# Performance work log

Measured on AMD Instinct MI355X. Metric: run time of the kernel, lower is better.

## Reference

```python
import jax, jax.numpy as jnp
import numpy as np

# Quantization configuration mirroring the module-level constants in the source
INPUT_BIT, WEIGHT_BIT, OUTPUT_BIT, DAC_BIT, ADC_BIT = 8, 4, 8, 2, 8
N_SLICES = INPUT_BIT // DAC_BIT  # 4 bit-serial DAC slices of 2 bits each


def ste_round(v):
    # straight-through estimator round (fake-quant / LSQ style)
    return v + jax.lax.stop_gradient(jnp.round(v) - v)


def setup_inputs() -> dict:
    key = jax.random.key(0)
    k1, k2, k3 = jax.random.split(key, 3)
    B, IN_F, OUT_F = 32768, 1024, 1024
    x = jax.random.normal(k1, (B, IN_F), jnp.float32)
    weight = jax.random.normal(k2, (OUT_F, IN_F), jnp.float32) * 0.02
    bias = jax.random.normal(k3, (OUT_F,), jnp.float32) * 0.01
    # LSQ step sizes (learned scalars) for input / weight / output fake-quant
    s_x = jnp.float32(4.0 / 255.0)
    s_w = jnp.float32(0.01)
    s_o = jnp.float32(0.05)
    # per-output-column ADC gain (adc_adjust_mode='gain'); noise scales are 0 -> deterministic
    gain = jnp.ones((OUT_F,), jnp.float32)
    return {"x": x, "weight": weight, "bias": bias, "s_x": s_x, "s_w": s_w, "s_o": s_o, "gain": gain}


def reference(x, weight, bias, s_x, s_w, s_o, gain):
    QP_IN = float(2 ** INPUT_BIT - 1)                      # unsigned 8-bit activations
    QN_W, QP_W = float(-2 ** (WEIGHT_BIT - 1)), float(2 ** (WEIGHT_BIT - 1) - 1)  # signed 4-bit weights
    QN_A, QP_A = float(-2 ** (ADC_BIT - 1)), float(2 ** (ADC_BIT - 1) - 1)        # 8-bit ADC
    QN_O, QP_O = float(-2 ** (OUTPUT_BIT - 1)), float(2 ** (OUTPUT_BIT - 1) - 1)  # signed 8-bit output

    # --- input / weight fake quantization (LSQ) ---
    x_int = ste_round(jnp.clip(x / s_x, 0.0, QP_IN))       # [B, in_f] integer codes (float dtype)
    w_int = ste_round(jnp.clip(weight / s_w, QN_W, QP_W))  # [out_f, in_f]

    # ideal integer matmul result (differentiable path)
    ideal = jnp.matmul(x_int, w_int.T) * (s_x * s_w)       # [B, out_f]

    # --- bit-serial DAC slicing + per-slice ADC (hardware emulation, non-diff) ---
    xi = jax.lax.stop_gradient(x_int)
    wi = jax.lax.stop_gradient(w_int)
    g = jax.lax.stop_gradient(gain)                        # [out_f]
    base = float(2 ** DAC_BIT)
    acc = jnp.zeros((x.shape[0], weight.shape[0]), x.dtype)
    for i in range(N_SLICES):  # fixed small loop (4 slices)
        shift = base ** i
        sl = jnp.mod(jnp.floor(xi / shift), base)          # 2-bit slice in {0,1,2,3}
        partial = jnp.matmul(sl, wi.T)                     # analog MAC result [B, out_f]
        adc = jnp.clip(jnp.round(partial * g), QN_A, QP_A) / g  # ADC quant with column gain
        acc = acc + adc * shift
    out_cim = acc * (s_x * s_w)

    # straight-through: forward value = CIM-emulated, gradient = ideal path
    out = ideal + jax.lax.stop_gradient(out_cim - ideal) + bias

    # --- output fake quantization ---
    y = s_o * ste_round(jnp.clip(out / s_o, QN_O, QP_O))
    return y
```

## Files before the change

kernel.cpp:

```cpp
#pragma float_control(precise, on)
#include <hip/hip_runtime.h>
#include <stdint.h>


typedef int i32x4 __attribute__((ext_vector_type(4)));

#define MDIM   32768
#define KDIM   1024
#define NDIM   1024
#define ABLK   131072
#define AKTS   8192
#define BBLK   262144
#define BKTS   16384

__device__ __forceinline__ void gload16(const void* g, void* l) {
  __builtin_amdgcn_global_load_lds(
      (const __attribute__((address_space(1))) void*)g,
      (__attribute__((address_space(3))) void*)l,
      16, 0, 0);
}

__global__ __launch_bounds__(256) void quant_x_kernel(
    const float* __restrict__ x, const float* __restrict__ s_x_p,
    uint8_t* __restrict__ Aq, uint8_t* __restrict__ rowFlag) {
  const float rcp = 1.0f / s_x_p[0];
  const int tid = blockIdx.x * 256 + threadIdx.x;
  const int m   = tid >> 6;
  const int k16 = tid & 63;
  const float* xp = x + (size_t)m * KDIM + k16 * 16;
  float vv[16];
#pragma unroll
  for (int q = 0; q < 4; ++q) {
    const float4 v = *(const float4*)(xp + q * 4);
    vv[q * 4 + 0] = v.x; vv[q * 4 + 1] = v.y; vv[q * 4 + 2] = v.z; vv[q * 4 + 3] = v.w;
  }
  int c[16];
  bool anyAmb = false;
#pragma unroll
  for (int j = 0; j < 16; ++j) {
    const float t  = vv[j] * rcp;
    const float tc = fminf(fmaxf(t, 0.0f), 255.0f);
    const float kf = rintf(tc);
    c[j] = (int)kf;
    const float d = 0.5f - fabsf(tc - kf);
    anyAmb = anyAmb || (d < 4e-7f * (tc + 1.0f));
  }
  if (anyAmb) rowFlag[m] = 1;
  const int bm  = m >> 5;
  const int g   = (m >> 2) & 7;
  const int fr4 = (m & 3) * 4;
  const int kt  = k16 >> 2, kl = k16 & 3;
  uint8_t* base = Aq + (size_t)bm * ABLK + kt * AKTS + (g << 10) + (kl * 16 + fr4) * 16;
#pragma unroll
  for (int s = 0; s < 4; ++s) {
    uint32_t w[4];
#pragma unroll
    for (int q = 0; q < 4; ++q) {
      w[q] =  (uint32_t)((c[q*4+0] >> (2*s)) & 3)
           | ((uint32_t)((c[q*4+1] >> (2*s)) & 3) << 8)
           | ((uint32_t)((c[q*4+2] >> (2*s)) & 3) << 16)
           | ((uint32_t)((c[q*4+3] >> (2*s)) & 3) << 24);
    }
    *(uint4*)(base + s * 16) = make_uint4(w[0], w[1], w[2], w[3]);
  }
}

__global__ __launch_bounds__(256) void quant_w_kernel(
    const float* __restrict__ wgt, const float* __restrict__ s_w_p,
    uint8_t* __restrict__ Bq, int* __restrict__ colInfo) {
  const float rcp = 1.0f / s_w_p[0];
  const int tid = blockIdx.x * 256 + threadIdx.x;
  const int n   = tid >> 6;
  const int k16 = tid & 63;
  const float* wp = wgt + (size_t)n * KDIM + k16 * 16;
  float vv[16];
#pragma unroll
  for (int q = 0; q < 4; ++q) {
    const float4 v = *(const float4*)(wp + q * 4);
    vv[q * 4 + 0] = v.x; vv[q * 4 + 1] = v.y; vv[q * 4 + 2] = v.z; vv[q * 4 + 3] = v.w;
  }
  uint32_t w[4];
#pragma unroll
  for (int q = 0; q < 4; ++q) w[q] = 0;
#pragma unroll
  for (int j = 0; j < 16; ++j) {
    const float t  = vv[j] * rcp;
    const float tc = fminf(fmaxf(t, -8.0f), 7.0f);
    const float kf = rintf(tc);
    const int   iv = (int)kf;
    const float fr = tc - kf;
    const float d  = 0.5f - fabsf(fr);
    if (d < 4e-7f * (fabsf(tc) + 1.0f)) {
      const int jj = k16 * 16 + j;
      colInfo[n] = (jj << 2) | ((fr > 0.0f) ? 2 : 0) | 1;
    }
    w[j >> 2] |= (uint32_t)((uint8_t)iv) << (8 * (j & 3));
  }
  const int bn  = n >> 8;
  const int rr  = n & 255;
  const int g   = rr >> 4;
  const int fr_ = rr & 15;
  const int kt  = k16 >> 2, kl = k16 & 3;
  uint8_t* dst = Bq + (size_t)bn * BBLK + kt * BKTS + (g << 10) + (kl * 16 + fr_) * 16;
  *(uint4*)dst = make_uint4(w[0], w[1], w[2], w[3]);
}

struct ChainOut { float kf; float tc; };
__device__ __forceinline__ ChainOut cim_chain(float p0, float p1, float p2, float p3,
                                              float bi, float sxsw, float rcp_so) {
#pragma clang fp contract(off)
  const float a0 = fminf(fmaxf(p0, -128.f), 127.f);
  const float a1 = fminf(fmaxf(p1, -128.f), 127.f);
  const float a2 = fminf(fmaxf(p2, -128.f), 127.f);
  const float a3 = fminf(fmaxf(p3, -128.f), 127.f);
  float acc_i = a0 + a1 * 4.f;
  acc_i = acc_i + a2 * 16.f;
  acc_i = acc_i + a3 * 64.f;
  float idl_i = p0 + p1 * 4.f;
  idl_i = idl_i + p2 * 16.f;
  idl_i = idl_i + p3 * 64.f;
  const float cim  = acc_i * sxsw;
  const float idea = idl_i * sxsw;
  float ov = idea + (cim - idea);
  ov = ov + bi;
  const float t  = ov * rcp_so;
  const float tc = fminf(fmaxf(t, -128.f), 127.f);
  ChainOut r; r.kf = rintf(tc); r.tc = tc; return r;
}

__global__ __launch_bounds__(512, 4) void gemm_cim(
    const uint8_t* __restrict__ Aq, const uint8_t* __restrict__ Bq,
    const float* __restrict__ bias, const float* __restrict__ gain,
    const float* __restrict__ s_x_p, const float* __restrict__ s_w_p,
    const float* __restrict__ s_o_p, const uint8_t* __restrict__ rowFlag,
    const int* __restrict__ colInfo, float* __restrict__ C) {
  __shared__ uint8_t sA[3][8192];
  __shared__ uint8_t sB[3][16384];

  const int t    = threadIdx.x;
  const int l    = ((int)blockIdx.x & 7) * 512 + ((int)blockIdx.x >> 3);
  const int bn   = l & 3;
  const int bm   = l >> 2;
  const int lane = t & 63;
  const int wv   = t >> 6;
  const int wr   = wv >> 2, wc = wv & 3;
  const int fr   = lane & 15, lk = lane >> 4;

  const uint8_t* gA = Aq + (size_t)bm * ABLK;
  const uint8_t* gB = Bq + (size_t)bn * BBLK;

  i32x4 acc[4][4];
#pragma unroll
  for (int i = 0; i < 4; ++i)
#pragma unroll
    for (int j = 0; j < 4; ++j) acc[i][j] = (i32x4){0, 0, 0, 0};

  const int lofs = lane * 16;
  const int o0 = t * 16, o1 = t * 16 + 8192;

  auto STAGE_ALL = [&](int kt, int bf) {
    gload16(gA + kt * AKTS + o0, sA[bf] + o0);
    gload16(gB + kt * BKTS + o0, sB[bf] + o0);
    gload16(gB + kt * BKTS + o1, sB[bf] + o1);
  };

  STAGE_ALL(0, 0);
  STAGE_ALL(1, 1);

  for (int kt = 0; kt < 16; ++kt) {
    const int bf = kt % 3;
    const int pf = (kt + 2) % 3;
    if (kt < 15) asm volatile("s_waitcnt vmcnt(3)" ::: "memory");
    else         asm volatile("s_waitcnt vmcnt(0)" ::: "memory");
    __builtin_amdgcn_sched_barrier(0);
    __builtin_amdgcn_s_barrier();
    if (kt + 2 < 16) STAGE_ALL(kt + 2, pf);

    i32x4 b0 = *(const i32x4*)(sB[bf] + ((wc * 4 + 0) << 10) + lofs);
    i32x4 b1 = *(const i32x4*)(sB[bf] + ((wc * 4 + 1) << 10) + lofs);
    i32x4 b2 = *(const i32x4*)(sB[bf] + ((wc * 4 + 2) << 10) + lofs);
    i32x4 b3 = *(const i32x4*)(sB[bf] + ((wc * 4 + 3) << 10) + lofs);
    __builtin_amdgcn_s_setprio(1);
#pragma unroll
    for (int mi = 0; mi < 4; ++mi) {
      i32x4 a = *(const i32x4*)(sA[bf] + ((wr * 4 + mi) << 10) + lofs);
      acc[mi][0] = __builtin_amdgcn_mfma_i32_16x16x64_i8(a, b0, acc[mi][0], 0, 0, 0);
      acc[mi][1] = __builtin_amdgcn_mfma_i32_16x16x64_i8(a, b1, acc[mi][1], 0, 0, 0);
      acc[mi][2] = __builtin_amdgcn_mfma_i32_16x16x64_i8(a, b2, acc[mi][2], 0, 0, 0);
      acc[mi][3] = __builtin_amdgcn_mfma_i32_16x16x64_i8(a, b3, acc[mi][3], 0, 0, 0);
    }
    __builtin_amdgcn_s_setprio(0);
  }

  {
#pragma clang fp contract(off)
    const float sxf = s_x_p[0], swf = s_w_p[0], sof = s_o_p[0];
    const float sxsw   = sxf * swf;
    const float rcp_so = 1.0f / sof;
#pragma unroll
    for (int ni = 0; ni < 4; ++ni) {
      const int   col = bn * 256 + wc * 64 + ni * 16 + fr;
      const float g   = gain[col];
      const float bi  = bias[col];
      const int   ci  = colInfo[col];
#pragma unroll
      for (int mi = 0; mi < 4; ++mi) {
        const int rowA = bm * 128 + wr * 64 + mi * 16 + lk * 4;
        const int m    = rowA >> 2;
        const i32x4 pi = acc[mi][ni];
        const float p0 = (float)pi[0], p1 = (float)pi[1];
        const float p2 = (float)pi[2], p3 = (float)pi[3];
        float y;
        if (g == 1.0f) {
          const ChainOut c0 = cim_chain(p0, p1, p2, p3, bi, sxsw, rcp_so);
          bool done = false;
          if (ci & 1) {
            const int   jj  = ci >> 2;
            const float dir = (ci & 2) ? 1.f : -1.f;
            const uint8_t* ab = Aq + (size_t)(m >> 5) * ABLK + (jj >> 6) * AKTS
                                + (((m >> 2) & 7) << 10)
                                + ((((jj >> 4) & 3) * 16 + (m & 3) * 4) * 16) + (jj & 15);
            const float q0 = (float)ab[0];
            const float q1 = (float)ab[16];
            const float q2 = (float)ab[32];
            const float q3 = (float)ab[48];
            const ChainOut c1 = cim_chain(p0 + dir * q0, p1 + dir * q1,
                                          p2 + dir * q2, p3 + dir * q3,
                                          bi, sxsw, rcp_so);
            if (c1.kf != c0.kf) {
              y = sof * (0.5f * (c0.kf + c1.kf));
              done = true;
            }
          }
          if (!done) {
            const float frac = c0.tc - c0.kf;
            const float d    = 0.5f - fabsf(frac);
            const float eps  = rowFlag[m] ? 0.03f : 1e-3f;
            if (d < eps && frac != 0.0f)
              y = sof * (c0.kf + ((frac > 0.0f) ? 0.5f : -0.5f));
            else
              y = sof * c0.kf;
          }
        } else {
          float a0 = fminf(fmaxf(rintf(p0 * g), -128.f), 127.f) / g;
          float a1 = fminf(fmaxf(rintf(p1 * g), -128.f), 127.f) / g;
          float a2 = fminf(fmaxf(rintf(p2 * g), -128.f), 127.f) / g;
          float a3 = fminf(fmaxf(rintf(p3 * g), -128.f), 127.f) / g;
          float acc_i = ((a0 + a1 * 4.f) + a2 * 16.f) + a3 * 64.f;
          float idl_i = ((p0 + p1 * 4.f) + p2 * 16.f) + p3 * 64.f;
          float ov = idl_i * sxsw + (acc_i * sxsw - idl_i * sxsw) + bi;
          float tc = fminf(fmaxf(ov * rcp_so, -128.f), 127.f);
          y = sof * rintf(tc);
        }
        C[(size_t)m * NDIM + col] = y;
      }
    }
  }
}

extern "C" void kernel_launch(void* const* d_in, const int* in_sizes, int n_in,
                              void* d_out, int out_size, void* d_ws, size_t ws_size,
                              hipStream_t stream) {
  const float* x    = (const float*)d_in[0];
  const float* wgt  = (const float*)d_in[1];
  const float* bias = (const float*)d_in[2];
  const float* s_x  = (const float*)d_in[3];
  const float* s_w  = (const float*)d_in[4];
  const float* s_o  = (const float*)d_in[5];
  const float* gain = (const float*)d_in[6];
  float* C = (float*)d_out;

  const size_t aq_bytes = (size_t)1024 * ABLK;
  const size_t bq_bytes = (size_t)4 * BBLK;
  const size_t fl_bytes = MDIM + NDIM * sizeof(int);
  if (ws_size < aq_bytes + bq_bytes + fl_bytes) return;

  uint8_t* Aq      = (uint8_t*)d_ws;
  uint8_t* Bq      = Aq + aq_bytes;
  uint8_t* rowFlag = Bq + bq_bytes;
  int*     colInfo = (int*)(rowFlag + MDIM);

  hipMemsetAsync(rowFlag, 0, fl_bytes, stream);
  quant_x_kernel<<<dim3(8192), dim3(256), 0, stream>>>(x, s_x, Aq, rowFlag);
  quant_w_kernel<<<dim3(256),  dim3(256), 0, stream>>>(wgt, s_w, Bq, colInfo);
  gemm_cim<<<dim3(4096), dim3(512), 0, stream>>>(Aq, Bq, bias, gain, s_x, s_w, s_o,
                                                 rowFlag, colInfo, C);
}
```

Measured before the change: 252.5 us.

## Switch int8 GEMM to 32x32x32 MFMA tiles with matching operand layout

The GEMM inner loop moves from 16x16x64 int8 MFMA to 32x32x32 int8 MFMA, with 2x2 accumulator tiles per wave instead of 4x4. The quantization kernels now write A and B in a packed layout that matches the new fragment shapes, and the epilogue is re-indexed to the 32x32 output layout, including the lookup of A values used for tie-breaking. The larger MFMA is meant to give more compute per LDS operand load and fewer instructions per k-step. The cost is different register use for the accumulators and more LDS fragment loads issued before the MFMAs begin.

```diff
diff --git a/kernel.cpp b/kernel.cpp
--- a/kernel.cpp
+++ b/kernel.cpp
@@ -3,7 +3,8 @@
 #include <stdint.h>
 
 
-typedef int i32x4 __attribute__((ext_vector_type(4)));
+typedef int i32x4  __attribute__((ext_vector_type(4)));
+typedef int i32x16 __attribute__((ext_vector_type(16)));
 
 #define MDIM   32768
 #define KDIM   1024
@@ -46,11 +47,14 @@
     anyAmb = anyAmb || (d < 4e-7f * (tc + 1.0f));
   }
   if (anyAmb) rowFlag[m] = 1;
-  const int bm  = m >> 5;
-  const int g   = (m >> 2) & 7;
-  const int fr4 = (m & 3) * 4;
-  const int kt  = k16 >> 2, kl = k16 & 3;
-  uint8_t* base = Aq + (size_t)bm * ABLK + kt * AKTS + (g << 10) + (kl * 16 + fr4) * 16;
+  const int mm    = m & 31;
+  const int mfrag = mm >> 3;
+  const int rowb  = 4 * (mm & 7);
+  const int kt    = k16 >> 2;
+  const int khalf = (k16 >> 1) & 1;
+  const int ksub  = k16 & 1;
+  uint8_t* base = Aq + (size_t)(m >> 5) * ABLK + kt * AKTS
+                  + ((mfrag * 2 + khalf) << 10) + (rowb + 32 * ksub) * 16;
 #pragma unroll
   for (int s = 0; s < 4; ++s) {
     uint32_t w[4];
@@ -96,12 +100,14 @@
     }
     w[j >> 2] |= (uint32_t)((uint8_t)iv) << (8 * (j & 3));
   }
-  const int bn  = n >> 8;
-  const int rr  = n & 255;
-  const int g   = rr >> 4;
-  const int fr_ = rr & 15;
-  const int kt  = k16 >> 2, kl = k16 & 3;
-  uint8_t* dst = Bq + (size_t)bn * BBLK + kt * BKTS + (g << 10) + (kl * 16 + fr_) * 16;
+  const int nn    = n & 255;
+  const int nfrag = nn >> 5;
+  const int colr  = nn & 31;
+  const int kt    = k16 >> 2;
+  const int khalf = (k16 >> 1) & 1;
+  const int ksub  = k16 & 1;
+  uint8_t* dst = Bq + (size_t)(n >> 8) * BBLK + kt * BKTS
+                 + ((nfrag * 2 + khalf) << 10) + (colr + 32 * ksub) * 16;
   *(uint4*)dst = make_uint4(w[0], w[1], w[2], w[3]);
 }
 
@@ -144,16 +150,15 @@
   const int lane = t & 63;
   const int wv   = t >> 6;
   const int wr   = wv >> 2, wc = wv & 3;
-  const int fr   = lane & 15, lk = lane >> 4;
 
   const uint8_t* gA = Aq + (size_t)bm * ABLK;
   const uint8_t* gB = Bq + (size_t)bn * BBLK;
 
-  i32x4 acc[4][4];
-#pragma unroll
-  for (int i = 0; i < 4; ++i)
-#pragma unroll
-    for (int j = 0; j < 4; ++j) acc[i][j] = (i32x4){0, 0, 0, 0};
+  i32x16 acc[2][2];
+#pragma unroll
+  for (int i = 0; i < 2; ++i)
+#pragma unroll
+    for (int j = 0; j < 2; ++j) acc[i][j] = (i32x16){0};
 
   const int lofs = lane * 16;
   const int o0 = t * 16, o1 = t * 16 + 8192;
@@ -176,19 +181,27 @@
     __builtin_amdgcn_s_barrier();
     if (kt + 2 < 16) STAGE_ALL(kt + 2, pf);
 
-    i32x4 b0 = *(const i32x4*)(sB[bf] + ((wc * 4 + 0) << 10) + lofs);
-    i32x4 b1 = *(const i32x4*)(sB[bf] + ((wc * 4 + 1) << 10) + lofs);
-    i32x4 b2 = *(const i32x4*)(sB[bf] + ((wc * 4 + 2) << 10) + lofs);
-    i32x4 b3 = *(const i32x4*)(sB[bf] + ((wc * 4 + 3) << 10) + lofs);
+    i32x4 a[2][2], b[2][2];
+#pragma unroll
+    for (int mf = 0; mf < 2; ++mf)
+#pragma unroll
+      for (int kh = 0; kh < 2; ++kh)
+        a[mf][kh] = *(const i32x4*)(sA[bf] + (((wr * 2 + mf) * 2 + kh) << 10) + lofs);
+#pragma unroll
+    for (int nf = 0; nf < 2; ++nf)
+#pragma unroll
+      for (int kh = 0; kh < 2; ++kh)
+        b[nf][kh] = *(const i32x4*)(sB[bf] + (((wc * 2 + nf) * 2 + kh) << 10) + lofs);
+
     __builtin_amdgcn_s_setprio(1);
 #pragma unroll
-    for (int mi = 0; mi < 4; ++mi) {
-      i32x4 a = *(const i32x4*)(sA[bf] + ((wr * 4 + mi) << 10) + lofs);
-      acc[mi][0] = __builtin_amdgcn_mfma_i32_16x16x64_i8(a, b0, acc[mi][0], 0, 0, 0);
-      acc[mi][1] = __builtin_amdgcn_mfma_i32_16x16x64_i8(a, b1, acc[mi][1], 0, 0, 0);
-      acc[mi][2] = __builtin_amdgcn_mfma_i32_16x16x64_i8(a, b2, acc[mi][2], 0, 0, 0);
-      acc[mi][3] = __builtin_amdgcn_mfma_i32_16x16x64_i8(a, b3, acc[mi][3], 0, 0, 0);
-    }
+    for (int kh = 0; kh < 2; ++kh)
+#pragma unroll
+      for (int mf = 0; mf < 2; ++mf)
+#pragma unroll
+        for (int nf = 0; nf < 2; ++nf)
+          acc[mf][nf] = __builtin_amdgcn_mfma_i32_32x32x32_i8(
+              a[mf][kh], b[nf][kh], acc[mf][nf], 0, 0, 0);
     __builtin_amdgcn_s_setprio(0);
   }
 
@@ -197,62 +210,67 @@
     const float sxf = s_x_p[0], swf = s_w_p[0], sof = s_o_p[0];
     const float sxsw   = sxf * swf;
     const float rcp_so = 1.0f / sof;
-#pragma unroll
-    for (int ni = 0; ni < 4; ++ni) {
-      const int   col = bn * 256 + wc * 64 + ni * 16 + fr;
+    const int   lc  = lane & 31;
+    const int   lh  = lane >> 5;
+#pragma unroll
+    for (int nf = 0; nf < 2; ++nf) {
+      const int   col = bn * 256 + wc * 64 + nf * 32 + lc;
       const float g   = gain[col];
       const float bi  = bias[col];
       const int   ci  = colInfo[col];
 #pragma unroll
-      for (int mi = 0; mi < 4; ++mi) {
-        const int rowA = bm * 128 + wr * 64 + mi * 16 + lk * 4;
-        const int m    = rowA >> 2;
-        const i32x4 pi = acc[mi][ni];
-        const float p0 = (float)pi[0], p1 = (float)pi[1];
-        const float p2 = (float)pi[2], p3 = (float)pi[3];
-        float y;
-        if (g == 1.0f) {
-          const ChainOut c0 = cim_chain(p0, p1, p2, p3, bi, sxsw, rcp_so);
-          bool done = false;
-          if (ci & 1) {
-            const int   jj  = ci >> 2;
-            const float dir = (ci & 2) ? 1.f : -1.f;
-            const uint8_t* ab = Aq + (size_t)(m >> 5) * ABLK + (jj >> 6) * AKTS
-                                + (((m >> 2) & 7) << 10)
-                                + ((((jj >> 4) & 3) * 16 + (m & 3) * 4) * 16) + (jj & 15);
-            const float q0 = (float)ab[0];
-            const float q1 = (float)ab[16];
-            const float q2 = (float)ab[32];
-            const float q3 = (float)ab[48];
-            const ChainOut c1 = cim_chain(p0 + dir * q0, p1 + dir * q1,
-                                          p2 + dir * q2, p3 + dir * q3,
-                                          bi, sxsw, rcp_so);
-            if (c1.kf != c0.kf) {
-              y = sof * (0.5f * (c0.kf + c1.kf));
-              done = true;
+      for (int mf = 0; mf < 2; ++mf) {
+#pragma unroll
+        for (int q = 0; q < 4; ++q) {
+          const int m = bm * 32 + wr * 16 + mf * 8 + 2 * q + lh;
+          const float p0 = (float)acc[mf][nf][4 * q + 0];
+          const float p1 = (float)acc[mf][nf][4 * q + 1];
+          const float p2 = (float)acc[mf][nf][4 * q + 2];
+          const float p3 = (float)acc[mf][nf][4 * q + 3];
+          float y;
+          if (g == 1.0f) {
+            const ChainOut c0 = cim_chain(p0, p1, p2, p3, bi, sxsw, rcp_so);
+            bool done = false;
+            if (ci & 1) {
+              const int   jj  = ci >> 2;
+              const float dir = (ci & 2) ? 1.f : -1.f;
+              const uint8_t* ab = Aq + (size_t)(m >> 5) * ABLK + (jj >> 6) * AKTS
+                  + ((((m & 31) >> 3) * 2 + ((jj >> 5) & 1)) << 10)
+                  + ((4 * (m & 7) + 32 * ((jj >> 4) & 1)) * 16) + (jj & 15);
+              const float q0 = (float)ab[0];
+              const float q1 = (float)ab[16];
+              const float q2 = (float)ab[32];
+              const float q3 = (float)ab[48];
+              const ChainOut c1 = cim_chain(p0 + dir * q0, p1 + dir * q1,
+                                            p2 + dir * q2, p3 + dir * q3,
+                                            bi, sxsw, rcp_so);
+              if (c1.kf != c0.kf) {
+                y = sof * (0.5f * (c0.kf + c1.kf));
+                done = true;
+              }
             }
+            if (!done) {
+              const float frac = c0.tc - c0.kf;
+              const float d    = 0.5f - fabsf(frac);
+              const float eps  = rowFlag[m] ? 0.03f : 1e-3f;
+              if (d < eps && frac != 0.0f)
+                y = sof * (c0.kf + ((frac > 0.0f) ? 0.5f : -0.5f));
+              else
+                y = sof * c0.kf;
+            }
+          } else {
+            float a0 = fminf(fmaxf(rintf(p0 * g), -128.f), 127.f) / g;
+            float a1 = fminf(fmaxf(rintf(p1 * g), -128.f), 127.f) / g;
+            float a2 = fminf(fmaxf(rintf(p2 * g), -128.f), 127.f) / g;
+            float a3 = fminf(fmaxf(rintf(p3 * g), -128.f), 127.f) / g;
+            float acc_i = ((a0 + a1 * 4.f) + a2 * 16.f) + a3 * 64.f;
+            float idl_i = ((p0 + p1 * 4.f) + p2 * 16.f) + p3 * 64.f;
+            float ov = idl_i * sxsw + (acc_i * sxsw - idl_i * sxsw) + bi;
+            float tc = fminf(fmaxf(ov * rcp_so, -128.f), 127.f);
+            y = sof * rintf(tc);
           }
-          if (!done) {
-            const float frac = c0.tc - c0.kf;
-            const float d    = 0.5f - fabsf(frac);
-            const float eps  = rowFlag[m] ? 0.03f : 1e-3f;
-            if (d < eps && frac != 0.0f)
-              y = sof * (c0.kf + ((frac > 0.0f) ? 0.5f : -0.5f));
-            else
-              y = sof * c0.kf;
-          }
-        } else {
-          float a0 = fminf(fmaxf(rintf(p0 * g), -128.f), 127.f) / g;
-          float a1 = fminf(fmaxf(rintf(p1 * g), -128.f), 127.f) / g;
-          float a2 = fminf(fmaxf(rintf(p2 * g), -128.f), 127.f) / g;
-          float a3 = fminf(fmaxf(rintf(p3 * g), -128.f), 127.f) / g;
-          float acc_i = ((a0 + a1 * 4.f) + a2 * 16.f) + a3 * 64.f;
-          float idl_i = ((p0 + p1 * 4.f) + p2 * 16.f) + p3 * 64.f;
-          float ov = idl_i * sxsw + (acc_i * sxsw - idl_i * sxsw) + bi;
-          float tc = fminf(fmaxf(ov * rcp_so, -128.f), 127.f);
-          y = sof * rintf(tc);
+          C[(size_t)m * NDIM + col] = y;
         }
-        C[(size_t)m * NDIM + col] = y;
       }
     }
   }
```

New measurement: 274.5 us. 8.7% more time.
